# Kernel optimization log

Measured on AMD Instinct MI355X. Metric: run time of the kernel, lower is better.

## Reference

```python
import jax, jax.numpy as jnp
import numpy as np

STRIDE = 1
PAD = 1
EXTENT = 3  # kernel footprint (ceil of max tap offset), 3x3 tap grid


def setup_inputs() -> dict:
    key = jax.random.key(0)
    k1, k2 = jax.random.split(key)
    B, Cin, H, W = 8, 64, 128, 128
    Cout, K = 64, 9
    x = jax.random.normal(k1, (B, Cin, H, W), dtype=jnp.float32)
    # per-tap weights, one scalar weight per (out_ch, in_ch, tap) -- op formula is 'x * w'
    weights = jax.random.normal(k2, (Cout, Cin, K), dtype=jnp.float32) * 0.05
    # 3x3 integer grid shifted by +0.4 -> non-integer offsets => bilinear (sub-pixel) gather
    base = jnp.stack(jnp.meshgrid(jnp.arange(3.0), jnp.arange(3.0), indexing='ij'), -1).reshape(9, 2)
    tap_offsets = (base + 0.4).astype(jnp.float32)  # [K, 2] (dy, dx)
    return {"x": x, "weights": weights, "tap_offsets": tap_offsets}


def _bilinear_tap(xp, dy, dx, H_out, W_out):
    # Gather xp at (oy*stride + dy, ox*stride + dx) with separable bilinear interp.
    Hp, Wp = xp.shape[-2], xp.shape[-1]
    y = jnp.arange(H_out, dtype=xp.dtype) * STRIDE + dy
    xc = jnp.arange(W_out, dtype=xp.dtype) * STRIDE + dx
    y0 = jnp.floor(y)
    x0 = jnp.floor(xc)
    fy = (y - y0)[None, None, :, None]
    fx = (xc - x0)[None, None, None, :]
    y0i = jnp.clip(y0.astype(jnp.int32), 0, Hp - 1)
    y1i = jnp.clip(y0.astype(jnp.int32) + 1, 0, Hp - 1)
    x0i = jnp.clip(x0.astype(jnp.int32), 0, Wp - 1)
    x1i = jnp.clip(x0.astype(jnp.int32) + 1, 0, Wp - 1)
    # interp rows first: [B, C, H_out, Wp]
    ry = xp[:, :, y0i, :] * (1.0 - fy) + xp[:, :, y1i, :] * fy
    # then columns: [B, C, H_out, W_out]
    return ry[:, :, :, x0i] * (1.0 - fx) + ry[:, :, :, x1i] * fx


def reference(x, weights, tap_offsets):
    B, Cin, H, W = x.shape
    K = weights.shape[-1]
    xp = jnp.pad(x, ((0, 0), (0, 0), (PAD, PAD), (PAD, PAD)))
    H_out = (H + 2 * PAD - EXTENT) // STRIDE + 1
    W_out = (W + 2 * PAD - EXTENT) // STRIDE + 1
    # gather all taps (loop over small fixed K=9, each fully vectorized over B,C,H,W)
    taps = [_bilinear_tap(xp, tap_offsets[k, 0], tap_offsets[k, 1], H_out, W_out)
            for k in range(K)]
    g = jnp.stack(taps, 0)  # [K, B, Cin, H_out, W_out]
    # per-tap op 'x * w', accumulated over taps and input channels
    return jnp.einsum('kbiyx,oik->boyx', g, weights)  # [B, Cout, H_out, W_out]
```

## Files before the change

kernel.cpp:

```cpp
#include <hip/hip_runtime.h>


#define CIN   64
#define COUT  64
#define HH    128
#define WW    128
#define NC    68

typedef __attribute__((ext_vector_type(8))) short bf16x8;
typedef __attribute__((ext_vector_type(4))) float f32x4;
typedef __attribute__((ext_vector_type(4))) unsigned int u32x4;

__device__ __forceinline__ unsigned short f2bf(float f) {
  unsigned int u = __float_as_uint(f);
  u = (u + 0x7fffu + ((u >> 16) & 1u)) >> 16;
  return (unsigned short)u;
}

__device__ __forceinline__ unsigned int cvtpk(float lo, float hi) {
  unsigned int r;
  asm("v_cvt_pk_bf16_f32 %0, %1, %2" : "=v"(r) : "v"(lo), "v"(hi));
  return r;
}

__global__ void make_wb(const float* __restrict__ wgt,
                        const float* __restrict__ off,
                        unsigned short* __restrict__ wb2)
{
  int id = blockIdx.x * 64 + threadIdx.x;
  int o = id >> 6, c = id & 63;
  float W16[16];
  #pragma unroll
  for (int i = 0; i < 16; ++i) W16[i] = 0.f;
  for (int k = 0; k < 9; ++k) {
    float dy = off[2*k], dx = off[2*k+1];
    float fyf = floorf(dy), fxf = floorf(dx);
    int   iy = (int)fyf,   ix = (int)fxf;
    float fy = dy - fyf,   fx = dx - fxf;
    float wk = wgt[(o*CIN + c)*9 + k];
    W16[(iy  )*4 + ix  ] += wk * (1.f-fy)*(1.f-fx);
    W16[(iy  )*4 + ix+1] += wk * (1.f-fy)*fx;
    W16[(iy+1)*4 + ix  ] += wk * fy*(1.f-fx);
    W16[(iy+1)*4 + ix+1] += wk * fy*fx;
  }
  int p = c >> 5, q = (c >> 3) & 3, j = c & 7;
  int n = o >> 4, m15 = o & 15;
  int lanei = q*16 + m15;
  for (int rs = 0; rs < 16; ++rs)
    wb2[(size_t)(((p*16 + rs)*4 + n)*64 + lanei)*8 + j] = f2bf(W16[rs]);
}

__global__ __launch_bounds__(256, 8)
void conv_mfma(const float* __restrict__ x,
               const unsigned short* __restrict__ wb2,
               float* __restrict__ out)
{
  __shared__ __align__(16) unsigned short tile[4 * NC * 32];

  const int wg  = blockIdx.x;
  const int xcd = wg & 7;
  const int i   = wg >> 3;
  const int b   = i >> 5;
  const int r5  = i & 31;
  const int y0  = xcd * 16 + (r5 >> 1);
  const int x0  = (r5 & 1) * 64;
  const int t    = threadIdx.x;
  const int wave = t >> 6;
  const int lane = t & 63;
  const int m15  = lane & 15;
  const int q    = lane >> 4;
  const int wv   = __builtin_amdgcn_readfirstlane(wave);

  int gx   = x0 - 1 + lane;
  bool gxv = ((unsigned)gx < (unsigned)WW);
  int gxc  = gx < 0 ? 0 : (gx > WW-1 ? WW-1 : gx);
  int gxh  = x0 + 63 + lane;
  bool gxhv = ((unsigned)gxh < (unsigned)WW);
  int gxhc = gxh < 0 ? 0 : (gxh > WW-1 ? WW-1 : gxh);

  const int w4 = (lane >> 2) & 3;
  char* pst = (char*)tile + lane*64 + ((wv + w4) & 3)*16;

  const char* aptr[4];
  #pragma unroll
  for (int s = 0; s < 4; ++s) {
    int c0   = m15 + s;
    int slot = (q + (c0 >> 2)) & 3;
    aptr[s] = (const char*)tile + c0*64 + slot*16;
  }

  f32x4 acc[4];
  #pragma unroll
  for (int mi = 0; mi < 4; ++mi)
    acc[mi] = (f32x4){0.f, 0.f, 0.f, 0.f};

  #pragma unroll
  for (int p = 0; p < 2; ++p) {
    if (p) __syncthreads();

    #pragma unroll
    for (int it = 0; it < 4; ++it) {
      const int gy = y0 + it - 1;
      char* dst = pst + it*4352;
      if ((unsigned)gy < (unsigned)HH) {
        const float* ps = x + ((size_t)((b*CIN + p*32 + wv*8)*HH + gy))*WW;
        float v[8];
        #pragma unroll
        for (int cc = 0; cc < 8; ++cc) v[cc] = ps[(size_t)cc*HH*WW + gxc];
        unsigned int pk[4];
        #pragma unroll
        for (int ii = 0; ii < 4; ++ii) {
          pk[ii] = cvtpk(v[2*ii], v[2*ii+1]);
          pk[ii] = gxv ? pk[ii] : 0u;
        }
        *(u32x4*)dst = *(u32x4*)pk;
        if (lane < 3) {
          float vh[8];
          #pragma unroll
          for (int cc = 0; cc < 8; ++cc) vh[cc] = ps[(size_t)cc*HH*WW + gxhc];
          unsigned int ph[4];
          #pragma unroll
          for (int ii = 0; ii < 4; ++ii) {
            ph[ii] = cvtpk(vh[2*ii], vh[2*ii+1]);
            ph[ii] = gxhv ? ph[ii] : 0u;
          }
          *(u32x4*)(dst + 4096) = *(u32x4*)ph;
        }
      } else if (p == 0) {
        *(u32x4*)dst = (u32x4){0u,0u,0u,0u};
        if (lane < 3) *(u32x4*)(dst + 4096) = (u32x4){0u,0u,0u,0u};
      }
    }
    __syncthreads();

    const char* wp = (const char*)wb2 + (size_t)p*65536 + wv*1024 + (size_t)lane*16;
    __builtin_amdgcn_s_setprio(1);
    #pragma unroll
    for (int rs = 0; rs < 16; ++rs) {
      const int r = rs >> 2, s = rs & 3;
      bf16x8 bfr = *(const bf16x8*)(wp + rs*4096);
      bf16x8 afr[4];
      #pragma unroll
      for (int mi = 0; mi < 4; ++mi)
        afr[mi] = *(const bf16x8*)(aptr[s] + r*4352 + mi*1024);
      #pragma unroll
      for (int mi = 0; mi < 4; ++mi)
        acc[mi] = __builtin_amdgcn_mfma_f32_16x16x32_bf16(afr[mi], bfr, acc[mi], 0, 0, 0);
    }
    __builtin_amdgcn_s_setprio(0);
  }

  const int o = wave*16 + m15;
  float* orow = out + (((size_t)(b*COUT + o))*HH + y0)*WW + x0 + q*4;
  #pragma unroll
  for (int mi = 0; mi < 4; ++mi)
    *(f32x4*)&orow[mi*16] = acc[mi];
}

extern "C" void kernel_launch(void* const* d_in, const int* in_sizes, int n_in,
                              void* d_out, int out_size, void* d_ws, size_t ws_size,
                              hipStream_t stream)
{
  const float* x   = (const float*)d_in[0];
  const float* wgt = (const float*)d_in[1];
  const float* off = (const float*)d_in[2];
  float* out = (float*)d_out;
  unsigned short* wb2 = (unsigned short*)d_ws;

  make_wb<<<64, 64, 0, stream>>>(wgt, off, wb2);
  conv_mfma<<<2048, 256, 0, stream>>>(x, wb2, out);
}
```

Measured before the change: 109.7 us.

## Use single-wave workgroups with register-prefetched double-buffered LDS pipeline

Restructures the conv kernel from 4 waves per block (each owning 16 output channels) to one wave per block that computes all 64 output channels with a 4x4 MFMA accumulator grid. The input halo rows are streamed one row and channel-half at a time: the next row is loaded into registers while the current one is computed from a double-buffered LDS slice. This removes block-level barriers, and the output is staged through LDS so stores are coalesced. The cost is much higher register pressure (64 accumulators plus 64 prefetch floats), lower occupancy, and each wave issuing 4x more weight loads per A fragment.

After: 106.7 us. 1.03x faster.

```diff
diff --git a/kernel.cpp b/kernel.cpp
--- a/kernel.cpp
+++ b/kernel.cpp
@@ -5,7 +5,6 @@
 #define COUT  64
 #define HH    128
 #define WW    128
-#define NC    68
 
 typedef __attribute__((ext_vector_type(8))) short bf16x8;
 typedef __attribute__((ext_vector_type(4))) float f32x4;
@@ -50,12 +49,12 @@
     wb2[(size_t)(((p*16 + rs)*4 + n)*64 + lanei)*8 + j] = f2bf(W16[rs]);
 }
 
-__global__ __launch_bounds__(256, 8)
+__global__ __launch_bounds__(64, 2)
 void conv_mfma(const float* __restrict__ x,
                const unsigned short* __restrict__ wb2,
                float* __restrict__ out)
 {
-  __shared__ __align__(16) unsigned short tile[4 * NC * 32];
+  __shared__ __align__(16) char lds[17408];
 
   const int wg  = blockIdx.x;
   const int xcd = wg & 7;
@@ -64,97 +63,130 @@
   const int r5  = i & 31;
   const int y0  = xcd * 16 + (r5 >> 1);
   const int x0  = (r5 & 1) * 64;
-  const int t    = threadIdx.x;
-  const int wave = t >> 6;
-  const int lane = t & 63;
+  const int lane = threadIdx.x;
   const int m15  = lane & 15;
   const int q    = lane >> 4;
-  const int wv   = __builtin_amdgcn_readfirstlane(wave);
 
   int gx   = x0 - 1 + lane;
   bool gxv = ((unsigned)gx < (unsigned)WW);
   int gxc  = gx < 0 ? 0 : (gx > WW-1 ? WW-1 : gx);
-  int gxh  = x0 + 63 + lane;
-  bool gxhv = ((unsigned)gxh < (unsigned)WW);
-  int gxhc = gxh < 0 ? 0 : (gxh > WW-1 ? WW-1 : gxh);
-
-  const int w4 = (lane >> 2) & 3;
-  char* pst = (char*)tile + lane*64 + ((wv + w4) & 3)*16;
-
-  const char* aptr[4];
+  const int he = (lane >> 4) < 3 ? (lane >> 4) : 2;
+  int gxh  = x0 + 63 + he;
+  bool gxhv = ((unsigned)gxh < (unsigned)WW) && (lane < 48);
+  int gxhc = gxh > WW-1 ? WW-1 : gxh;
+  const int hp = lane & 15;
+  const int hoff = (64 + he)*64 + ((hp >> 2) & 3)*16 + (hp & 3)*4;
+
+  int stoff[4];
+  #pragma unroll
+  for (int c = 0; c < 4; ++c)
+    stoff[c] = lane*64 + ((c + (lane >> 2)) & 3)*16;
+
+  int aoff[4];
   #pragma unroll
   for (int s = 0; s < 4; ++s) {
-    int c0   = m15 + s;
-    int slot = (q + (c0 >> 2)) & 3;
-    aptr[s] = (const char*)tile + c0*64 + slot*16;
-  }
-
-  f32x4 acc[4];
+    int c0 = m15 + s;
+    aoff[s] = c0*64 + ((q + (c0 >> 2)) & 3)*16;
+  }
+
+  f32x4 acc[4][4];
   #pragma unroll
   for (int mi = 0; mi < 4; ++mi)
-    acc[mi] = (f32x4){0.f, 0.f, 0.f, 0.f};
-
-  #pragma unroll
-  for (int p = 0; p < 2; ++p) {
-    if (p) __syncthreads();
-
     #pragma unroll
-    for (int it = 0; it < 4; ++it) {
-      const int gy = y0 + it - 1;
-      char* dst = pst + it*4352;
-      if ((unsigned)gy < (unsigned)HH) {
-        const float* ps = x + ((size_t)((b*CIN + p*32 + wv*8)*HH + gy))*WW;
-        float v[8];
-        #pragma unroll
-        for (int cc = 0; cc < 8; ++cc) v[cc] = ps[(size_t)cc*HH*WW + gxc];
+    for (int nn = 0; nn < 4; ++nn)
+      acc[mi][nn] = (f32x4){0.f, 0.f, 0.f, 0.f};
+
+  float GM0[32], GM1[32], GH0[2], GH1[2];
+
+  auto LOADP = [&](int k, float* GM, float* GH) {
+    int gy = y0 + (k & 3) - 1;
+    if ((unsigned)gy < (unsigned)HH) {
+      const float* ps = x + ((size_t)((b*CIN + (k >> 2)*32)*HH + gy))*WW;
+      #pragma unroll
+      for (int cc = 0; cc < 32; ++cc) GM[cc] = ps[(size_t)cc*HH*WW + gxc];
+      GH[0] = ps[(size_t)(2*hp    )*HH*WW + gxhc];
+      GH[1] = ps[(size_t)(2*hp + 1)*HH*WW + gxhc];
+    }
+  };
+
+  auto WRITEP = [&](int k, const float* GM, const float* GH) {
+    int gy = y0 + (k & 3) - 1;
+    char* base = lds + (k & 1)*4352;
+    if ((unsigned)gy < (unsigned)HH) {
+      #pragma unroll
+      for (int c = 0; c < 4; ++c) {
         unsigned int pk[4];
         #pragma unroll
-        for (int ii = 0; ii < 4; ++ii) {
-          pk[ii] = cvtpk(v[2*ii], v[2*ii+1]);
-          pk[ii] = gxv ? pk[ii] : 0u;
+        for (int w = 0; w < 4; ++w) {
+          pk[w] = cvtpk(GM[c*8 + 2*w], GM[c*8 + 2*w + 1]);
+          pk[w] = gxv ? pk[w] : 0u;
         }
-        *(u32x4*)dst = *(u32x4*)pk;
-        if (lane < 3) {
-          float vh[8];
-          #pragma unroll
-          for (int cc = 0; cc < 8; ++cc) vh[cc] = ps[(size_t)cc*HH*WW + gxhc];
-          unsigned int ph[4];
-          #pragma unroll
-          for (int ii = 0; ii < 4; ++ii) {
-            ph[ii] = cvtpk(vh[2*ii], vh[2*ii+1]);
-            ph[ii] = gxhv ? ph[ii] : 0u;
-          }
-          *(u32x4*)(dst + 4096) = *(u32x4*)ph;
-        }
-      } else if (p == 0) {
-        *(u32x4*)dst = (u32x4){0u,0u,0u,0u};
-        if (lane < 3) *(u32x4*)(dst + 4096) = (u32x4){0u,0u,0u,0u};
+        *(u32x4*)(base + stoff[c]) = *(u32x4*)pk;
       }
-    }
-    __syncthreads();
-
-    const char* wp = (const char*)wb2 + (size_t)p*65536 + wv*1024 + (size_t)lane*16;
-    __builtin_amdgcn_s_setprio(1);
+      unsigned int hw = cvtpk(GH[0], GH[1]);
+      hw = gxhv ? hw : 0u;
+      if (lane < 48) *(unsigned int*)(base + hoff) = hw;
+    } else {
+      #pragma unroll
+      for (int c = 0; c < 4; ++c)
+        *(u32x4*)(base + stoff[c]) = (u32x4){0u,0u,0u,0u};
+      if (lane < 48) *(unsigned int*)(base + hoff) = 0u;
+    }
+  };
+
+  auto COMPUTE = [&](int k) {
+    const char* wpB = (const char*)wb2 + (size_t)(k >> 2)*65536 + (size_t)lane*16;
+    const char* ab  = lds + (k & 1)*4352;
+    const int r4 = (k & 3)*4;
     #pragma unroll
-    for (int rs = 0; rs < 16; ++rs) {
-      const int r = rs >> 2, s = rs & 3;
-      bf16x8 bfr = *(const bf16x8*)(wp + rs*4096);
-      bf16x8 afr[4];
+    for (int s = 0; s < 4; ++s) {
+      const char* wrow = wpB + (size_t)(r4 + s)*4096;
+      bf16x8 bfr[4], afr[4];
+      #pragma unroll
+      for (int n = 0; n < 4; ++n)
+        bfr[n] = *(const bf16x8*)(wrow + n*1024);
       #pragma unroll
       for (int mi = 0; mi < 4; ++mi)
-        afr[mi] = *(const bf16x8*)(aptr[s] + r*4352 + mi*1024);
+        afr[mi] = *(const bf16x8*)(ab + aoff[s] + mi*1024);
       #pragma unroll
       for (int mi = 0; mi < 4; ++mi)
-        acc[mi] = __builtin_amdgcn_mfma_f32_16x16x32_bf16(afr[mi], bfr, acc[mi], 0, 0, 0);
-    }
-    __builtin_amdgcn_s_setprio(0);
-  }
-
-  const int o = wave*16 + m15;
-  float* orow = out + (((size_t)(b*COUT + o))*HH + y0)*WW + x0 + q*4;
+        #pragma unroll
+        for (int nn = 0; nn < 4; ++nn)
+          acc[mi][nn] = __builtin_amdgcn_mfma_f32_16x16x32_bf16(afr[mi], bfr[nn], acc[mi][nn], 0, 0, 0);
+    }
+  };
+
+  LOADP(0, GM0, GH0);
+  LOADP(1, GM1, GH1);
+  WRITEP(0, GM0, GH0);
+  #pragma unroll
+  for (int kk = 0; kk < 4; ++kk) {
+    if (kk < 3) LOADP(2*kk + 2, GM0, GH0);
+    WRITEP(2*kk + 1, GM1, GH1);
+    COMPUTE(2*kk);
+    if (kk < 3) {
+      LOADP(2*kk + 3, GM1, GH1);
+      WRITEP(2*kk + 2, GM0, GH0);
+    }
+    COMPUTE(2*kk + 1);
+  }
+
+  float* epi = (float*)lds;
   #pragma unroll
   for (int mi = 0; mi < 4; ++mi)
-    *(f32x4*)&orow[mi*16] = acc[mi];
+    #pragma unroll
+    for (int nn = 0; nn < 4; ++nn) {
+      int o  = nn*16 + m15;
+      int px = mi*16 + q*4;
+      *(f32x4*)&epi[o*68 + px] = acc[mi][nn];
+    }
+  #pragma unroll
+  for (int i2 = 0; i2 < 16; ++i2) {
+    int o  = i2*4 + q;
+    int px = m15*4;
+    f32x4 v = *(const f32x4*)&epi[o*68 + px];
+    *(f32x4*)&out[(((size_t)(b*COUT + o))*HH + y0)*WW + x0 + px] = v;
+  }
 }
 
 extern "C" void kernel_launch(void* const* d_in, const int* in_sizes, int n_in,
@@ -168,5 +200,5 @@
   unsigned short* wb2 = (unsigned short*)d_ws;
 
   make_wb<<<64, 64, 0, stream>>>(wgt, off, wb2);
-  conv_mfma<<<2048, 256, 0, stream>>>(x, wb2, out);
-}
+  conv_mfma<<<2048, 64, 0, stream>>>(x, wb2, out);
+}
```
